# Performance work log

Hardware: AMD Instinct MI355X
Metric: run time of the kernel (lower is better)

The kernel has to match this reference:

```python
import jax, jax.numpy as jnp
import numpy as np

N_NODES = 200000
MEM_DIM = 256
MSG_DIM = 256
BATCH = 2048


def _gru_cell(x, h, wih, whh, bih, bhh):
    # PyTorch GRUCell: gates stacked [r, z, n] along dim 0 of weights.
    gi = wih @ x + bih  # (3H,)
    gh = whh @ h + bhh  # (3H,)
    i_r, i_z, i_n = jnp.split(gi, 3)
    h_r, h_z, h_n = jnp.split(gh, 3)
    r = jax.nn.sigmoid(i_r + h_r)
    z = jax.nn.sigmoid(i_z + h_z)
    n = jnp.tanh(i_n + r * h_n)
    return (1.0 - z) * n + z * h


def setup_inputs() -> dict:
    key = jax.random.key(0)
    ks = jax.random.split(key, 12)
    memory = jax.random.normal(ks[0], (N_NODES, MEM_DIM), jnp.float32) * 0.1
    last_update = jnp.zeros((N_NODES,), jnp.float32)
    src_nodes = jax.random.randint(ks[1], (BATCH,), 0, N_NODES, dtype=jnp.int32)
    dst_nodes = jax.random.randint(ks[2], (BATCH,), 0, N_NODES, dtype=jnp.int32)
    edge_feat = jax.random.normal(ks[3], (BATCH, 3), jnp.float32)
    timestamps = jnp.sort(jax.random.uniform(ks[4], (BATCH,), jnp.float32) * 1e4)
    in1 = 2 * MEM_DIM + 3
    W1 = jax.random.normal(ks[5], (MSG_DIM, in1), jnp.float32) / np.sqrt(in1).astype(np.float32)
    b1 = jnp.zeros((MSG_DIM,), jnp.float32)
    W2 = jax.random.normal(ks[6], (MSG_DIM, MSG_DIM), jnp.float32) / np.sqrt(MSG_DIM).astype(np.float32)
    b2 = jnp.zeros((MSG_DIM,), jnp.float32)
    gru_wih = jax.random.normal(ks[7], (3 * MEM_DIM, MSG_DIM), jnp.float32) / np.sqrt(MEM_DIM).astype(np.float32)
    gru_whh = jax.random.normal(ks[8], (3 * MEM_DIM, MEM_DIM), jnp.float32) / np.sqrt(MEM_DIM).astype(np.float32)
    gru_bih = jnp.zeros((3 * MEM_DIM,), jnp.float32)
    gru_bhh = jnp.zeros((3 * MEM_DIM,), jnp.float32)
    return {
        'src_nodes': src_nodes, 'dst_nodes': dst_nodes,
        'edge_feat': edge_feat, 'timestamps': timestamps,
        'memory': memory, 'last_update': last_update,
        'W1': W1, 'b1': b1, 'W2': W2, 'b2': b2,
        'gru_wih': gru_wih, 'gru_whh': gru_whh,
        'gru_bih': gru_bih, 'gru_bhh': gru_bhh,
    }


def reference(src_nodes, dst_nodes, edge_feat, timestamps, memory, last_update,
              W1, b1, W2, b2, gru_wih, gru_whh, gru_bih, gru_bhh):
    # Vectorized message encoding from the PRE-update memory (as in source).
    src_mem = memory[src_nodes]                         # (B, D)
    dst_mem = memory[dst_nodes]                         # (B, D)
    x = jnp.concatenate([src_mem, dst_mem, edge_feat], axis=1)  # (B, 2D+3)
    h = jax.nn.relu(x @ W1.T + b1)
    messages = h @ W2.T + b2                            # (B, M)

    # Sequential per-event GRU scatter updates (read-after-write preserved).
    def step(carry, inp):
        mem, lu = carry
        s, d, msg, t = inp
        new_s = _gru_cell(msg, mem[s], gru_wih, gru_whh, gru_bih, gru_bhh)
        mem = mem.at[s].set(new_s)
        lu = lu.at[s].set(t)
        new_d = _gru_cell(msg, mem[d], gru_wih, gru_whh, gru_bih, gru_bhh)
        mem = mem.at[d].set(new_d)
        lu = lu.at[d].set(t)
        return (mem, lu), None

    (mem_out, lu_out), _ = jax.lax.scan(
        step, (memory, last_update), (src_nodes, dst_nodes, messages, timestamps))
    return mem_out, lu_out
```

## Files before the change

kernel.cpp:

```cpp
#include <hip/hip_runtime.h>
#include <hip/hip_bf16.h>
#include <math.h>
#include <limits.h>

#define N_NODES 200000
#define MEM_DIM 256
#define MSG_DIM 256
#define BATCH 2048
#define NSLOTS (2*BATCH)
#define IN1 515
#define K1PAD 528
#define G3 768

#define OFF_X      0
#define SZ_X       (BATCH*K1PAD)
#define OFF_W1P    (OFF_X + SZ_X)
#define SZ_W1P     (MSG_DIM*K1PAD)
#define OFF_HMID   (OFF_W1P + SZ_W1P)
#define SZ_HMID    (BATCH*MSG_DIM)
#define OFF_MSG    (OFF_HMID + SZ_HMID)
#define SZ_MSG     (BATCH*MSG_DIM)
#define OFF_PREGI  (OFF_MSG + SZ_MSG)
#define SZ_PREGI   (BATCH*G3)
#define OFF_WHHT   (OFF_PREGI + SZ_PREGI)
#define SZ_WHHT    (G3*MEM_DIM)
#define OFF_INTS   (OFF_WHHT + SZ_WHHT)

__global__ void pack_w1(const float* __restrict__ W1, float* __restrict__ W1p) {
    int i = blockIdx.x * 256 + threadIdx.x;
    if (i >= MSG_DIM * K1PAD) return;
    int n = i / K1PAD, k = i - n * K1PAD;
    W1p[i] = (k < IN1) ? W1[n * IN1 + k] : 0.f;
}

__global__ void build_x(const int* __restrict__ src, const int* __restrict__ dst,
                        const float* __restrict__ ef, const float* __restrict__ memory,
                        float* __restrict__ X) {
    int ev = blockIdx.x;
    int s = src[ev], d = dst[ev];
    const float* sm = memory + (long)s * MEM_DIM;
    const float* dm = memory + (long)d * MEM_DIM;
    float* x = X + (long)ev * K1PAD;
    for (int i = threadIdx.x; i < K1PAD; i += 256) {
        float v;
        if (i < 256)      v = sm[i];
        else if (i < 512) v = dm[i - 256];
        else if (i < 515) v = ef[ev * 3 + (i - 512)];
        else              v = 0.f;
        x[i] = v;
    }
}

__global__ void transpose_whh(const float* __restrict__ whh, float* __restrict__ whhT) {
    __shared__ float tile[32][33];
    int jb = blockIdx.x * 32;
    int kb = blockIdx.y * 32;
    int tx = threadIdx.x & 31, ty = threadIdx.x >> 5;
    #pragma unroll
    for (int r = 0; r < 32; r += 8)
        tile[ty + r][tx] = whh[(long)(jb + ty + r) * 256 + kb + tx];
    __syncthreads();
    #pragma unroll
    for (int r = 0; r < 32; r += 8)
        whhT[(long)(kb + ty + r) * G3 + jb + tx] = tile[tx][ty + r];
}

template<bool RELU>
__global__ void gemm_bias(const float* __restrict__ A, int lda,
                          const float* __restrict__ B, int ldb,
                          const float* __restrict__ bias,
                          float* __restrict__ C, int ldc, int K) {
    __shared__ float As[16][64];
    __shared__ float Bs[16][64];
    int m0 = blockIdx.x * 64, n0 = blockIdx.y * 64;
    int tid = threadIdx.x;
    int tm = tid >> 4, tn = tid & 15;
    int lr = tid >> 2, lq = tid & 3;
    float acc[4][4] = {};
    for (int k0 = 0; k0 < K; k0 += 16) {
        float4 av = *(const float4*)&A[(long)(m0 + lr) * lda + k0 + lq * 4];
        float4 bv = *(const float4*)&B[(long)(n0 + lr) * ldb + k0 + lq * 4];
        __syncthreads();
        As[lq * 4 + 0][lr] = av.x; As[lq * 4 + 1][lr] = av.y;
        As[lq * 4 + 2][lr] = av.z; As[lq * 4 + 3][lr] = av.w;
        Bs[lq * 4 + 0][lr] = bv.x; Bs[lq * 4 + 1][lr] = bv.y;
        Bs[lq * 4 + 2][lr] = bv.z; Bs[lq * 4 + 3][lr] = bv.w;
        __syncthreads();
        #pragma unroll
        for (int kk = 0; kk < 16; ++kk) {
            float4 a = *(const float4*)&As[kk][tm * 4];
            float4 b = *(const float4*)&Bs[kk][tn * 4];
            const float* ap = (const float*)&a;
            const float* bp = (const float*)&b;
            #pragma unroll
            for (int i = 0; i < 4; ++i)
                #pragma unroll
                for (int j = 0; j < 4; ++j)
                    acc[i][j] += ap[i] * bp[j];
        }
    }
    #pragma unroll
    for (int i = 0; i < 4; ++i) {
        int row = m0 + tm * 4 + i;
        float4 o;
        float* op = (float*)&o;
        #pragma unroll
        for (int j = 0; j < 4; ++j) {
            float v = acc[i][j] + bias[n0 + tn * 4 + j];
            if (RELU) v = fmaxf(v, 0.f);
            op[j] = v;
        }
        *(float4*)&C[(long)row * ldc + n0 + tn * 4] = o;
    }
}

#define ULB 4
__global__ void build_links(const int* __restrict__ src, const int* __restrict__ dst,
                            int* __restrict__ nodes, int* __restrict__ nxt,
                            int* __restrict__ head_list, int* __restrict__ head_count) {
    __shared__ int sn[NSLOTS];
    __shared__ int smin[ULB];
    __shared__ int searly[ULB];
    for (int i = threadIdx.x; i < NSLOTS; i += 256) {
        int ev = i >> 1;
        sn[i] = (i & 1) ? dst[ev] : src[ev];
    }
    if (threadIdx.x < ULB) { smin[threadIdx.x] = INT_MAX; searly[threadIdx.x] = 0; }
    __syncthreads();
    int u0 = blockIdx.x * ULB;
    int myn[ULB];
    #pragma unroll
    for (int c = 0; c < ULB; ++c) myn[c] = sn[u0 + c];
    int lmin[ULB]; int learly[ULB];
    #pragma unroll
    for (int c = 0; c < ULB; ++c) { lmin[c] = INT_MAX; learly[c] = 0; }
    for (int w = threadIdx.x; w < NSLOTS; w += 256) {
        int nw = sn[w];
        #pragma unroll
        for (int c = 0; c < ULB; ++c) {
            if (nw == myn[c]) {
                int u = u0 + c;
                if (w > u)      lmin[c] = min(lmin[c], w);
                else if (w < u) learly[c] = 1;
            }
        }
    }
    #pragma unroll
    for (int c = 0; c < ULB; ++c) {
        if (lmin[c] != INT_MAX) atomicMin(&smin[c], lmin[c]);
        if (learly[c])          atomicOr(&searly[c], 1);
    }
    __syncthreads();
    if (threadIdx.x < ULB) {
        int u = u0 + threadIdx.x;
        nodes[u] = myn[threadIdx.x];
        int nx = smin[threadIdx.x];
        nxt[u] = (nx == INT_MAX) ? -1 : nx;
        if (!searly[threadIdx.x]) {
            int p = atomicAdd(head_count, 1);
            head_list[p] = u;
        }
    }
}

__global__ void copy_out(const float4* __restrict__ mem4, const float4* __restrict__ lu4,
                         float4* __restrict__ out4) {
    const long NM4 = (long)N_NODES * MEM_DIM / 4;
    const long NT4 = NM4 + N_NODES / 4;
    for (long i = (long)blockIdx.x * 256 + threadIdx.x; i < NT4; i += (long)gridDim.x * 256)
        out4[i] = (i < NM4) ? mem4[i] : lu4[i - NM4];
}

#define CPB 8
__global__ void chain_kernel(const int* __restrict__ nodes, const int* __restrict__ nxt,
                             const int* __restrict__ head_list, const int* __restrict__ head_count,
                             const float* __restrict__ memory,
                             const float* __restrict__ pregi,
                             const float* __restrict__ whhT,
                             const float* __restrict__ bhh,
                             const float* __restrict__ ts,
                             float* __restrict__ out_mem, float* __restrict__ out_lu) {
    __shared__ __align__(16) float hs[CPB][MEM_DIM];
    int t = threadIdx.x;
    int hc = *head_count;
    int base = blockIdx.x * CPB;
    int u[CPB], v[CPB];
    float tl[CPB];
    bool any = false;
    #pragma unroll
    for (int c = 0; c < CPB; ++c) {
        int idx = base + c;
        if (idx < hc) { u[c] = head_list[idx]; v[c] = nodes[u[c]]; any = true; }
        else          { u[c] = -1; v[c] = -1; }
        tl[c] = 0.f;
    }
    if (!any) return;
    #pragma unroll
    for (int c = 0; c < CPB; ++c)
        hs[c][t] = (v[c] >= 0) ? memory[(long)v[c] * MEM_DIM + t] : 0.f;
    float bh0 = bhh[t], bh1 = bhh[256 + t], bh2 = bhh[512 + t];

    while (true) {
        bool act = false;
        #pragma unroll
        for (int c = 0; c < CPB; ++c) act = act || (u[c] >= 0);
        if (!act) break;
        __syncthreads();
        float a0[CPB], a1[CPB], a2[CPB];
        #pragma unroll
        for (int c = 0; c < CPB; ++c) { a0[c] = bh0; a1[c] = bh1; a2[c] = bh2; }
        for (int k = 0; k < MEM_DIM; k += 4) {
            float4 hv[CPB];
            #pragma unroll
            for (int c = 0; c < CPB; ++c) hv[c] = *(const float4*)&hs[c][k];
            #pragma unroll
            for (int q = 0; q < 4; ++q) {
                float w0 = whhT[(long)(k + q) * G3 + t];
                float w1 = whhT[(long)(k + q) * G3 + 256 + t];
                float w2 = whhT[(long)(k + q) * G3 + 512 + t];
                #pragma unroll
                for (int c = 0; c < CPB; ++c) {
                    float hk = ((const float*)&hv[c])[q];
                    a0[c] += hk * w0; a1[c] += hk * w1; a2[c] += hk * w2;
                }
            }
        }
        float hn[CPB];
        #pragma unroll
        for (int c = 0; c < CPB; ++c) {
            if (u[c] < 0) { hn[c] = 0.f; continue; }
            int ev = u[c] >> 1;
            float gi0 = pregi[(long)ev * G3 + t];
            float gi1 = pregi[(long)ev * G3 + 256 + t];
            float gi2 = pregi[(long)ev * G3 + 512 + t];
            float r = 1.f / (1.f + expf(-(gi0 + a0[c])));
            float z = 1.f / (1.f + expf(-(gi1 + a1[c])));
            float n = tanhf(gi2 + r * a2[c]);
            hn[c] = (1.f - z) * n + z * hs[c][t];
            tl[c] = ts[ev];
        }
        __syncthreads();
        #pragma unroll
        for (int c = 0; c < CPB; ++c)
            if (u[c] >= 0) { hs[c][t] = hn[c]; u[c] = nxt[u[c]]; }
    }
    #pragma unroll
    for (int c = 0; c < CPB; ++c) {
        if (v[c] < 0) continue;
        out_mem[(long)v[c] * MEM_DIM + t] = hs[c][t];
        if (t == 0) out_lu[v[c]] = tl[c];
    }
}

extern "C" void kernel_launch(void* const* d_in, const int* in_sizes, int n_in,
                              void* d_out, int out_size, void* d_ws, size_t ws_size,
                              hipStream_t stream) {
    (void)in_sizes; (void)n_in; (void)out_size; (void)ws_size;
    const int*   src    = (const int*)d_in[0];
    const int*   dst    = (const int*)d_in[1];
    const float* ef     = (const float*)d_in[2];
    const float* ts     = (const float*)d_in[3];
    const float* memory = (const float*)d_in[4];
    const float* lastup = (const float*)d_in[5];
    const float* W1     = (const float*)d_in[6];
    const float* b1     = (const float*)d_in[7];
    const float* W2     = (const float*)d_in[8];
    const float* b2     = (const float*)d_in[9];
    const float* wih    = (const float*)d_in[10];
    const float* whh    = (const float*)d_in[11];
    const float* bih    = (const float*)d_in[12];
    const float* bhh    = (const float*)d_in[13];

    float* ws    = (float*)d_ws;
    float* X     = ws + OFF_X;
    float* W1p   = ws + OFF_W1P;
    float* Hmid  = ws + OFF_HMID;
    float* msg   = ws + OFF_MSG;
    float* pregi = ws + OFF_PREGI;
    float* whhT  = ws + OFF_WHHT;
    int*   ints  = (int*)(ws + OFF_INTS);
    int* nodes = ints;
    int* nxt   = ints + NSLOTS;
    int* hlist = ints + 2 * NSLOTS;
    int* hcnt  = ints + 3 * NSLOTS;

    hipMemsetAsync(hcnt, 0, sizeof(int), stream);
    pack_w1<<<(SZ_W1P + 255) / 256, 256, 0, stream>>>(W1, W1p);
    build_x<<<BATCH, 256, 0, stream>>>(src, dst, ef, memory, X);
    transpose_whh<<<dim3(G3 / 32, MEM_DIM / 32), 256, 0, stream>>>(whh, whhT);
    gemm_bias<true><<<dim3(BATCH / 64, MSG_DIM / 64), 256, 0, stream>>>(
        X, K1PAD, W1p, K1PAD, b1, Hmid, MSG_DIM, K1PAD);
    gemm_bias<false><<<dim3(BATCH / 64, MSG_DIM / 64), 256, 0, stream>>>(
        Hmid, MSG_DIM, W2, MSG_DIM, b2, msg, MSG_DIM, MSG_DIM);
    gemm_bias<false><<<dim3(BATCH / 64, G3 / 64), 256, 0, stream>>>(
        msg, MSG_DIM, wih, MSG_DIM, bih, pregi, G3, MSG_DIM);
    build_links<<<NSLOTS / ULB, 256, 0, stream>>>(src, dst, nodes, nxt, hlist, hcnt);
    copy_out<<<2048, 256, 0, stream>>>((const float4*)memory, (const float4*)lastup,
                                       (float4*)d_out);
    chain_kernel<<<NSLOTS / CPB, 256, 0, stream>>>(
        nodes, nxt, hlist, hcnt, memory, pregi, whhT, bhh, ts,
        (float*)d_out, (float*)d_out + (long)N_NODES * MEM_DIM);
}
```

Measured before the change: 550.0 us.

## Fuse memory copy-out with chain GRU kernel using a touched-node bitmap

Merges the bulk copy of untouched memory and last_update rows into the chain GRU kernel so the latency-bound chain work overlaps the bandwidth-bound copy. Blocks first run their chains, then pull copy chunks from an atomic work counter. A bitmap built in build_links marks updated nodes so the copy skips their rows and avoids write races. This adds a bitmap read per element and an atomic per chunk, and it assumes the memset ordering of the counter and bitmap.

```diff
diff --git a/kernel.cpp b/kernel.cpp
--- a/kernel.cpp
+++ b/kernel.cpp
@@ -11,6 +11,7 @@
 #define IN1 515
 #define K1PAD 528
 #define G3 768
+#define NBMWORDS 6250
 
 #define OFF_X      0
 #define SZ_X       (BATCH*K1PAD)
@@ -117,7 +118,8 @@
 #define ULB 4
 __global__ void build_links(const int* __restrict__ src, const int* __restrict__ dst,
                             int* __restrict__ nodes, int* __restrict__ nxt,
-                            int* __restrict__ head_list, int* __restrict__ head_count) {
+                            int* __restrict__ head_list, int* __restrict__ head_count,
+                            unsigned int* __restrict__ bitmap) {
     __shared__ int sn[NSLOTS];
     __shared__ int smin[ULB];
     __shared__ int searly[ULB];
@@ -153,7 +155,9 @@
     __syncthreads();
     if (threadIdx.x < ULB) {
         int u = u0 + threadIdx.x;
-        nodes[u] = myn[threadIdx.x];
+        int me = myn[threadIdx.x];
+        nodes[u] = me;
+        atomicOr(&bitmap[me >> 5], 1u << (me & 31));
         int nx = smin[threadIdx.x];
         nxt[u] = (nx == INT_MAX) ? -1 : nx;
         if (!searly[threadIdx.x]) {
@@ -163,92 +167,126 @@
     }
 }
 
-__global__ void copy_out(const float4* __restrict__ mem4, const float4* __restrict__ lu4,
-                         float4* __restrict__ out4) {
+#define CPB 8
+#define NCHAIN_BLKS (NSLOTS / CPB)
+#define COPY_GRID 2048
+#define COPY_CHUNK 8192L
+__global__ void copy_chain(const int* __restrict__ nodes, const int* __restrict__ nxt,
+                           const int* __restrict__ head_list, const int* __restrict__ head_count,
+                           const unsigned int* __restrict__ bitmap,
+                           const float* __restrict__ memory,
+                           const float* __restrict__ pregi,
+                           const float* __restrict__ whhT,
+                           const float* __restrict__ bhh,
+                           const float* __restrict__ ts,
+                           const float* __restrict__ lastup,
+                           float* __restrict__ out_mem, float* __restrict__ out_lu,
+                           int* __restrict__ wctr) {
+    __shared__ __align__(16) float hs[CPB][MEM_DIM];
+    __shared__ int chunkBase;
+    int t = threadIdx.x;
+
+    if (blockIdx.x < NCHAIN_BLKS) {
+        int hc = *head_count;
+        int base = blockIdx.x * CPB;
+        if (base < hc) {
+            int u[CPB], v[CPB];
+            float tl[CPB];
+            #pragma unroll
+            for (int c = 0; c < CPB; ++c) {
+                int idx = base + c;
+                if (idx < hc) { u[c] = head_list[idx]; v[c] = nodes[u[c]]; }
+                else          { u[c] = -1; v[c] = -1; }
+                tl[c] = 0.f;
+            }
+            #pragma unroll
+            for (int c = 0; c < CPB; ++c)
+                hs[c][t] = (v[c] >= 0) ? memory[(long)v[c] * MEM_DIM + t] : 0.f;
+            float bh0 = bhh[t], bh1 = bhh[256 + t], bh2 = bhh[512 + t];
+
+            while (true) {
+                bool act = false;
+                #pragma unroll
+                for (int c = 0; c < CPB; ++c) act = act || (u[c] >= 0);
+                if (!act) break;
+                __syncthreads();
+                float a0[CPB], a1[CPB], a2[CPB];
+                #pragma unroll
+                for (int c = 0; c < CPB; ++c) { a0[c] = bh0; a1[c] = bh1; a2[c] = bh2; }
+                for (int k = 0; k < MEM_DIM; k += 4) {
+                    float4 hv[CPB];
+                    #pragma unroll
+                    for (int c = 0; c < CPB; ++c) hv[c] = *(const float4*)&hs[c][k];
+                    #pragma unroll
+                    for (int q = 0; q < 4; ++q) {
+                        float w0 = whhT[(long)(k + q) * G3 + t];
+                        float w1 = whhT[(long)(k + q) * G3 + 256 + t];
+                        float w2 = whhT[(long)(k + q) * G3 + 512 + t];
+                        #pragma unroll
+                        for (int c = 0; c < CPB; ++c) {
+                            float hk = ((const float*)&hv[c])[q];
+                            a0[c] += hk * w0; a1[c] += hk * w1; a2[c] += hk * w2;
+                        }
+                    }
+                }
+                float hn[CPB];
+                #pragma unroll
+                for (int c = 0; c < CPB; ++c) {
+                    if (u[c] < 0) { hn[c] = 0.f; continue; }
+                    int ev = u[c] >> 1;
+                    float gi0 = pregi[(long)ev * G3 + t];
+                    float gi1 = pregi[(long)ev * G3 + 256 + t];
+                    float gi2 = pregi[(long)ev * G3 + 512 + t];
+                    float r = 1.f / (1.f + expf(-(gi0 + a0[c])));
+                    float z = 1.f / (1.f + expf(-(gi1 + a1[c])));
+                    float n = tanhf(gi2 + r * a2[c]);
+                    hn[c] = (1.f - z) * n + z * hs[c][t];
+                    tl[c] = ts[ev];
+                }
+                __syncthreads();
+                #pragma unroll
+                for (int c = 0; c < CPB; ++c)
+                    if (u[c] >= 0) { hs[c][t] = hn[c]; u[c] = nxt[u[c]]; }
+            }
+            #pragma unroll
+            for (int c = 0; c < CPB; ++c) {
+                if (v[c] < 0) continue;
+                out_mem[(long)v[c] * MEM_DIM + t] = hs[c][t];
+                if (t == 0) out_lu[v[c]] = tl[c];
+            }
+        }
+    }
+
     const long NM4 = (long)N_NODES * MEM_DIM / 4;
     const long NT4 = NM4 + N_NODES / 4;
-    for (long i = (long)blockIdx.x * 256 + threadIdx.x; i < NT4; i += (long)gridDim.x * 256)
-        out4[i] = (i < NM4) ? mem4[i] : lu4[i - NM4];
-}
-
-#define CPB 8
-__global__ void chain_kernel(const int* __restrict__ nodes, const int* __restrict__ nxt,
-                             const int* __restrict__ head_list, const int* __restrict__ head_count,
-                             const float* __restrict__ memory,
-                             const float* __restrict__ pregi,
-                             const float* __restrict__ whhT,
-                             const float* __restrict__ bhh,
-                             const float* __restrict__ ts,
-                             float* __restrict__ out_mem, float* __restrict__ out_lu) {
-    __shared__ __align__(16) float hs[CPB][MEM_DIM];
-    int t = threadIdx.x;
-    int hc = *head_count;
-    int base = blockIdx.x * CPB;
-    int u[CPB], v[CPB];
-    float tl[CPB];
-    bool any = false;
-    #pragma unroll
-    for (int c = 0; c < CPB; ++c) {
-        int idx = base + c;
-        if (idx < hc) { u[c] = head_list[idx]; v[c] = nodes[u[c]]; any = true; }
-        else          { u[c] = -1; v[c] = -1; }
-        tl[c] = 0.f;
-    }
-    if (!any) return;
-    #pragma unroll
-    for (int c = 0; c < CPB; ++c)
-        hs[c][t] = (v[c] >= 0) ? memory[(long)v[c] * MEM_DIM + t] : 0.f;
-    float bh0 = bhh[t], bh1 = bhh[256 + t], bh2 = bhh[512 + t];
-
+    const float4* mem4 = (const float4*)memory;
+    const float4* lu4  = (const float4*)lastup;
+    float4* out4 = (float4*)out_mem;
     while (true) {
-        bool act = false;
-        #pragma unroll
-        for (int c = 0; c < CPB; ++c) act = act || (u[c] >= 0);
-        if (!act) break;
+        if (t == 0) chunkBase = atomicAdd(wctr, 1);
         __syncthreads();
-        float a0[CPB], a1[CPB], a2[CPB];
-        #pragma unroll
-        for (int c = 0; c < CPB; ++c) { a0[c] = bh0; a1[c] = bh1; a2[c] = bh2; }
-        for (int k = 0; k < MEM_DIM; k += 4) {
-            float4 hv[CPB];
-            #pragma unroll
-            for (int c = 0; c < CPB; ++c) hv[c] = *(const float4*)&hs[c][k];
-            #pragma unroll
-            for (int q = 0; q < 4; ++q) {
-                float w0 = whhT[(long)(k + q) * G3 + t];
-                float w1 = whhT[(long)(k + q) * G3 + 256 + t];
-                float w2 = whhT[(long)(k + q) * G3 + 512 + t];
-                #pragma unroll
-                for (int c = 0; c < CPB; ++c) {
-                    float hk = ((const float*)&hv[c])[q];
-                    a0[c] += hk * w0; a1[c] += hk * w1; a2[c] += hk * w2;
+        long c0 = (long)chunkBase * COPY_CHUNK;
+        __syncthreads();
+        if (c0 >= NT4) break;
+        long cend = c0 + COPY_CHUNK; if (cend > NT4) cend = NT4;
+        for (long i = c0 + t; i < cend; i += 256) {
+            if (i < NM4) {
+                int node = (int)(i >> 6);
+                if (!((bitmap[node >> 5] >> (node & 31)) & 1u))
+                    out4[i] = mem4[i];
+            } else {
+                long j4 = i - NM4;
+                float4 lv = lu4[j4];
+                const float* lp = (const float*)&lv;
+                int n0 = (int)(j4 * 4);
+                #pragma unroll
+                for (int e = 0; e < 4; ++e) {
+                    int n = n0 + e;
+                    if (!((bitmap[n >> 5] >> (n & 31)) & 1u))
+                        out_lu[n] = lp[e];
                 }
             }
         }
-        float hn[CPB];
-        #pragma unroll
-        for (int c = 0; c < CPB; ++c) {
-            if (u[c] < 0) { hn[c] = 0.f; continue; }
-            int ev = u[c] >> 1;
-            float gi0 = pregi[(long)ev * G3 + t];
-            float gi1 = pregi[(long)ev * G3 + 256 + t];
-            float gi2 = pregi[(long)ev * G3 + 512 + t];
-            float r = 1.f / (1.f + expf(-(gi0 + a0[c])));
-            float z = 1.f / (1.f + expf(-(gi1 + a1[c])));
-            float n = tanhf(gi2 + r * a2[c]);
-            hn[c] = (1.f - z) * n + z * hs[c][t];
-            tl[c] = ts[ev];
-        }
-        __syncthreads();
-        #pragma unroll
-        for (int c = 0; c < CPB; ++c)
-            if (u[c] >= 0) { hs[c][t] = hn[c]; u[c] = nxt[u[c]]; }
-    }
-    #pragma unroll
-    for (int c = 0; c < CPB; ++c) {
-        if (v[c] < 0) continue;
-        out_mem[(long)v[c] * MEM_DIM + t] = hs[c][t];
-        if (t == 0) out_lu[v[c]] = tl[c];
     }
 }
 
@@ -283,8 +321,10 @@
     int* nxt   = ints + NSLOTS;
     int* hlist = ints + 2 * NSLOTS;
     int* hcnt  = ints + 3 * NSLOTS;
-
-    hipMemsetAsync(hcnt, 0, sizeof(int), stream);
+    int* wctr  = ints + 3 * NSLOTS + 1;
+    unsigned int* bitmap = (unsigned int*)(ints + 3 * NSLOTS + 2);
+
+    hipMemsetAsync(hcnt, 0, (2 + NBMWORDS) * sizeof(int), stream);
     pack_w1<<<(SZ_W1P + 255) / 256, 256, 0, stream>>>(W1, W1p);
     build_x<<<BATCH, 256, 0, stream>>>(src, dst, ef, memory, X);
     transpose_whh<<<dim3(G3 / 32, MEM_DIM / 32), 256, 0, stream>>>(whh, whhT);
@@ -294,10 +334,8 @@
         Hmid, MSG_DIM, W2, MSG_DIM, b2, msg, MSG_DIM, MSG_DIM);
     gemm_bias<false><<<dim3(BATCH / 64, G3 / 64), 256, 0, stream>>>(
         msg, MSG_DIM, wih, MSG_DIM, bih, pregi, G3, MSG_DIM);
-    build_links<<<NSLOTS / ULB, 256, 0, stream>>>(src, dst, nodes, nxt, hlist, hcnt);
-    copy_out<<<2048, 256, 0, stream>>>((const float4*)memory, (const float4*)lastup,
-                                       (float4*)d_out);
-    chain_kernel<<<NSLOTS / CPB, 256, 0, stream>>>(
-        nodes, nxt, hlist, hcnt, memory, pregi, whhT, bhh, ts,
-        (float*)d_out, (float*)d_out + (long)N_NODES * MEM_DIM);
-}
+    build_links<<<NSLOTS / ULB, 256, 0, stream>>>(src, dst, nodes, nxt, hlist, hcnt, bitmap);
+    copy_chain<<<COPY_GRID, 256, 0, stream>>>(
+        nodes, nxt, hlist, hcnt, bitmap, memory, pregi, whhT, bhh, ts, lastup,
+        (float*)d_out, (float*)d_out + (long)N_NODES * MEM_DIM, wctr);
+}
```

Measured after the change: 534.2 us. -2.9%, faster.
